# Optimization experiments

Hardware: AMD Instinct MI355X
Metric: run time of the kernel (lower is better)

## Reference

```python
import jax, jax.numpy as jnp
import numpy as np

SIGMA = 1.0

def setup_inputs() -> dict:
    key = jax.random.key(0)
    k1, k2 = jax.random.split(key)
    z = jax.random.normal(k1, (8192, 1024), dtype=jnp.float32)
    expert_keys = jax.random.normal(k2, (4096, 1024), dtype=jnp.float32)
    return {"z": z, "expert_keys": expert_keys}

def reference(z, expert_keys):
    # squared euclidean distances [N, E] = |z|^2 + |e|^2 - 2 z.e
    z_sq = jnp.sum(z * z, axis=-1, keepdims=True)          # [N, 1]
    e_sq = jnp.sum(expert_keys * expert_keys, axis=-1)     # [E]
    dist2 = z_sq + e_sq[None, :] - 2.0 * (z @ expert_keys.T)
    dist2 = jnp.maximum(dist2, 0.0)
    similarity = jnp.exp(-dist2 / (2.0 * SIGMA ** 2))       # [N, E]
    weights = jax.nn.softmax(similarity, axis=-1)            # [N, E]
    weighted_expert = weights @ expert_keys                  # [N, D]
    return (similarity, weighted_expert)
```

## Files before the change

### kernel.cpp

```cpp
#include <hip/hip_runtime.h>
#include <stdint.h>


#define M_TOK 8192
#define N_EXP 4096
#define D_DIM 1024

typedef __attribute__((ext_vector_type(4))) float f32x4;
typedef __attribute__((ext_vector_type(8))) short short8;
typedef __attribute__((ext_vector_type(4))) unsigned short u16x4;
typedef unsigned short u16;
typedef unsigned int u32;

__device__ __forceinline__ u16 f32_to_bf16(float f) {
  u32 u = __builtin_bit_cast(u32, f);
  u += 0x7fff + ((u >> 16) & 1);
  return (u16)(u >> 16);
}

__device__ __forceinline__ void async16(const void* g, void* l) {
  __builtin_amdgcn_global_load_lds((__attribute__((address_space(1))) void*)(g),
                                   (__attribute__((address_space(3))) void*)(l),
                                   16, 0, 0);
}

__global__ __launch_bounds__(256) void prep_convert2(const float* __restrict__ zsrc,
                                                     const float* __restrict__ esrc,
                                                     u16* __restrict__ zdst,
                                                     u16* __restrict__ edst,
                                                     float* __restrict__ zsq,
                                                     float* __restrict__ esq) {
  int row = blockIdx.x;
  const float* src;
  u16* dst;
  float* sq;
  if (row < M_TOK) {
    src = zsrc + (size_t)row * D_DIM;
    dst = zdst + (size_t)row * D_DIM;
    sq = zsq + row;
  } else {
    int r = row - M_TOK;
    src = esrc + (size_t)r * D_DIM;
    dst = edst + (size_t)r * D_DIM;
    sq = esq + r;
  }
  int t = threadIdx.x;
  const float4 v = ((const float4*)src)[t];
  ushort4 h;
  h.x = f32_to_bf16(v.x); h.y = f32_to_bf16(v.y);
  h.z = f32_to_bf16(v.z); h.w = f32_to_bf16(v.w);
  ((ushort4*)dst)[t] = h;
  float p = v.x * v.x + v.y * v.y + v.z * v.z + v.w * v.w;
#pragma unroll
  for (int off = 1; off < 64; off <<= 1) p += __shfl_xor(p, off, 64);
  __shared__ float partial[4];
  if ((t & 63) == 0) partial[t >> 6] = p;
  __syncthreads();
  if (t == 0) *sq = partial[0] + partial[1] + partial[2] + partial[3];
}

__global__ __launch_bounds__(256) void transpose_bf16(const u16* __restrict__ src,
                                                      u16* __restrict__ dst) {
  __shared__ u16 tile[64][65];
  int e0 = blockIdx.x * 64;
  int d0 = blockIdx.y * 64;
  int t = threadIdx.x;
  int lr = t >> 4;
  int lc = (t & 15) * 4;
#pragma unroll
  for (int r8 = 0; r8 < 4; ++r8) {
    int row = lr + r8 * 16;
    ushort4 v = *(const ushort4*)(src + (size_t)(e0 + row) * D_DIM + d0 + lc);
    tile[row][lc + 0] = v.x; tile[row][lc + 1] = v.y;
    tile[row][lc + 2] = v.z; tile[row][lc + 3] = v.w;
  }
  __syncthreads();
#pragma unroll
  for (int r8 = 0; r8 < 4; ++r8) {
    int dl = lr + r8 * 16;
    ushort4 v;
    v.x = tile[lc + 0][dl]; v.y = tile[lc + 1][dl];
    v.z = tile[lc + 2][dl]; v.w = tile[lc + 3][dl];
    *(ushort4*)(dst + (size_t)(d0 + dl) * N_EXP + e0 + lc) = v;
  }
}

__global__ __launch_bounds__(256) void rowsum_reduce(const float* __restrict__ part,
                                                     float* __restrict__ rowsum) {
  int r = blockIdx.x * 256 + threadIdx.x;
  float s = 0.f;
#pragma unroll 8
  for (int j = 0; j < 128; ++j) s += part[(size_t)j * M_TOK + r];
  rowsum[r] = s;
}

template <int EPI>
__global__ __launch_bounds__(512, 4) void gemm_bt(const u16* __restrict__ A,
                                                  const u16* __restrict__ Bt,
                                                  int Mdim, int Ndim, int Kdim,
                                                  float* __restrict__ out, int ldo,
                                                  const float* __restrict__ a_sq,
                                                  const float* __restrict__ b_sq,
                                                  float* __restrict__ rs_part,
                                                  u16* __restrict__ wb,
                                                  const float* __restrict__ scale) {
  constexpr int BM = 128, BN = 128, BK = 64;
  __shared__ __align__(16) u16 smA[2 * BM * BK];
  __shared__ __align__(16) u16 smB[2 * BN * BK];
  __shared__ float inv_rs[BM];

  const int wg = blockIdx.x;
  int m0, n0, ntile = 0;
  if (EPI == 1) {
    const int xcd = wg & 7;
    const int idx = wg >> 3;
    const int sup = idx >> 5;
    const int mloc = (idx & 31) >> 2;
    const int nloc = idx & 3;
    m0 = (xcd * 8 + mloc) * BM;
    ntile = sup * 4 + nloc;
    n0 = ntile * BN;
  } else {
    const int nTilesN = Ndim / BN;
    const int nwg = (Mdim / BM) * nTilesN;
    const int cpx = nwg >> 3;
    const int swz = (wg & 7) * cpx + (wg >> 3);
    m0 = (swz / nTilesN) * BM;
    n0 = (swz % nTilesN) * BN;
  }

  const int t = threadIdx.x;
  const int l = t & 63;
  const int w = t >> 6;
  const int wr = w >> 2;
  const int wc = w & 3;
  const int lr8 = l >> 3;
  const int cswz = (((l & 7) ^ lr8) << 3);
  const int s0 = w * 2, s1 = w * 2 + 1;
  const int str0 = s0 * 8 + lr8, str1 = s1 * 8 + lr8;

  f32x4 acc[4][2];
#pragma unroll
  for (int i = 0; i < 4; ++i)
#pragma unroll
    for (int j = 0; j < 2; ++j) acc[i][j] = (f32x4){0.f, 0.f, 0.f, 0.f};

  const int nIter = Kdim / BK;
  async16(A + (size_t)(m0 + str0) * Kdim + cswz, smA + s0 * 512);
  async16(A + (size_t)(m0 + str1) * Kdim + cswz, smA + s1 * 512);
  async16(Bt + (size_t)(n0 + str0) * Kdim + cswz, smB + s0 * 512);
  async16(Bt + (size_t)(n0 + str1) * Kdim + cswz, smB + s1 * 512);

  if (EPI == 0 && rs_part != nullptr) {
    const int rrow = t >> 2;
    const int q = t & 3;
    float s = 0.f;
#pragma unroll 8
    for (int j = q * 32; j < q * 32 + 32; ++j)
      s += rs_part[(size_t)j * M_TOK + m0 + rrow];
    s += __shfl_xor(s, 1, 64);
    s += __shfl_xor(s, 2, 64);
    if (q == 0) inv_rs[rrow] = 1.0f / s;
  }
  __syncthreads();

  int cur = 0;
  for (int it = 0; it < nIter; ++it) {
    if (it + 1 < nIter) {
      const int k0 = (it + 1) * BK;
      const int nb = (cur ^ 1) * 8192;
      async16(A + (size_t)(m0 + str0) * Kdim + k0 + cswz, smA + nb + s0 * 512);
      async16(A + (size_t)(m0 + str1) * Kdim + k0 + cswz, smA + nb + s1 * 512);
      async16(Bt + (size_t)(n0 + str0) * Kdim + k0 + cswz, smB + nb + s0 * 512);
      async16(Bt + (size_t)(n0 + str1) * Kdim + k0 + cswz, smB + nb + s1 * 512);
    }
    const int cbase = cur * 8192;
#pragma unroll
    for (int ks = 0; ks < 2; ++ks) {
      short8 af[4], bf[2];
      const int lrow = l & 15;
      const int kb = ks * 64 + ((l >> 4) << 4);
#pragma unroll
      for (int mi = 0; mi < 4; ++mi) {
        int row = wr * 64 + mi * 16 + lrow;
        int addr = row * 128 + (kb ^ ((row & 7) << 4));
        af[mi] = *(const short8*)(smA + cbase + (addr >> 1));
      }
#pragma unroll
      for (int ni = 0; ni < 2; ++ni) {
        int row = wc * 32 + ni * 16 + lrow;
        int addr = row * 128 + (kb ^ ((row & 7) << 4));
        bf[ni] = *(const short8*)(smB + cbase + (addr >> 1));
      }
#pragma unroll
      for (int mi = 0; mi < 4; ++mi)
#pragma unroll
        for (int ni = 0; ni < 2; ++ni)
          acc[mi][ni] = __builtin_amdgcn_mfma_f32_16x16x32_bf16(
              bf[ni], af[mi], acc[mi][ni], 0, 0, 0);
    }
    __syncthreads();
    cur ^= 1;
  }

  const int lcol = l & 15;
  const int rgrp = l >> 4;
  if (EPI == 1) {
    float* ldsT = ((float*)smA) + w * (16 * 36);
    const int rr = l >> 3;
    const int c4 = (l & 7) * 4;
    const int slot = ntile * 4 + wc;
#pragma unroll
    for (int mi = 0; mi < 4; ++mi) {
      int grow = m0 + wr * 64 + mi * 16 + lcol;
      float zq = a_sq[grow];
#pragma unroll
      for (int ni = 0; ni < 2; ++ni) {
        int ncol = n0 + wc * 32 + ni * 16 + rgrp * 4;
        f32x4 eqv = *(const f32x4*)(b_sq + ncol);
        f32x4 simv;
#pragma unroll
        for (int r = 0; r < 4; ++r) {
          float dist2 = fmaxf(zq + eqv[r] - 2.0f * acc[mi][ni][r], 0.0f);
          simv[r] = __expf(-0.5f * dist2);
        }
        *(f32x4*)(ldsT + lcol * 36 + ni * 16 + rgrp * 4) = simv;
      }
      asm volatile("s_waitcnt lgkmcnt(0)" ::: "memory");
#pragma unroll
      for (int pass = 0; pass < 2; ++pass) {
        int rrow = pass * 8 + rr;
        f32x4 sv = *(const f32x4*)(ldsT + rrow * 36 + c4);
        int growr = m0 + wr * 64 + mi * 16 + rrow;
        size_t gbase = (size_t)growr * ldo + (n0 + wc * 32 + c4);
        __builtin_nontemporal_store(sv, (f32x4*)(out + gbase));
        f32x4 es;
#pragma unroll
        for (int r = 0; r < 4; ++r) es[r] = __expf(sv[r]);
        if (wb) {
          u16x4 wv;
          wv.x = f32_to_bf16(es[0]); wv.y = f32_to_bf16(es[1]);
          wv.z = f32_to_bf16(es[2]); wv.w = f32_to_bf16(es[3]);
          *(u16x4*)(wb + gbase) = wv;
        }
        float p = es[0] + es[1] + es[2] + es[3];
        p += __shfl_xor(p, 1, 64);
        p += __shfl_xor(p, 2, 64);
        p += __shfl_xor(p, 4, 64);
        if ((l & 7) == 0) rs_part[(size_t)slot * M_TOK + growr] = p;
      }
    }
  } else {
#pragma unroll
    for (int mi = 0; mi < 4; ++mi) {
      int grow = m0 + wr * 64 + mi * 16 + lcol;
      float s;
      if (rs_part != nullptr)      s = inv_rs[wr * 64 + mi * 16 + lcol];
      else if (scale != nullptr)   s = 1.0f / scale[grow];
      else                         s = 1.0f;
#pragma unroll
      for (int ni = 0; ni < 2; ++ni) {
        int ncol = n0 + wc * 32 + ni * 16 + rgrp * 4;
        f32x4 v = acc[mi][ni] * s;
        *(f32x4*)(out + (size_t)grow * ldo + ncol) = v;
      }
    }
  }
}

__global__ __launch_bounds__(256) void weights_kernel(const float* __restrict__ sim,
                                                      const float* __restrict__ rowsum,
                                                      u16* __restrict__ wb) {
  size_t i = ((size_t)blockIdx.x * 256 + threadIdx.x) * 8;
  int row = (int)(i >> 12);
  float inv = 1.0f / rowsum[row];
  float4 a = *(const float4*)(sim + i);
  float4 b = *(const float4*)(sim + i + 4);
  u32 w0 = (u32)f32_to_bf16(__expf(a.x) * inv) | ((u32)f32_to_bf16(__expf(a.y) * inv) << 16);
  u32 w1 = (u32)f32_to_bf16(__expf(a.z) * inv) | ((u32)f32_to_bf16(__expf(a.w) * inv) << 16);
  u32 w2 = (u32)f32_to_bf16(__expf(b.x) * inv) | ((u32)f32_to_bf16(__expf(b.y) * inv) << 16);
  u32 w3 = (u32)f32_to_bf16(__expf(b.z) * inv) | ((u32)f32_to_bf16(__expf(b.w) * inv) << 16);
  uint4 o; o.x = w0; o.y = w1; o.z = w2; o.w = w3;
  *(uint4*)(wb + i) = o;
}

extern "C" void kernel_launch(void* const* d_in, const int* in_sizes, int n_in,
                              void* d_out, int out_size, void* d_ws, size_t ws_size,
                              hipStream_t stream) {
  const float* z = (const float*)d_in[0];
  const float* e = (const float*)d_in[1];
  float* out = (float*)d_out;
  float* sim = out;
  float* wout = out + (size_t)M_TOK * N_EXP;

  char* ws = (char*)d_ws;
  const size_t MB = (size_t)1 << 20;
  const bool fused = ws_size >= 100 * MB + 96 * 1024;

  if (fused) {
    u16* zb  = (u16*)ws;
    u16* eb  = (u16*)(ws + 16 * MB);
    u16* ebT = (u16*)(ws + 24 * MB);
    u16* Wb  = (u16*)(ws + 32 * MB);
    float* rs_part = (float*)(ws + 96 * MB);
    float* z_sq   = (float*)(ws + 100 * MB);
    float* e_sq   = (float*)(ws + 100 * MB + 32768);

    prep_convert2<<<M_TOK + N_EXP, 256, 0, stream>>>(z, e, zb, eb, z_sq, e_sq);
    transpose_bf16<<<dim3(N_EXP / 64, D_DIM / 64), 256, 0, stream>>>(eb, ebT);

    gemm_bt<1><<<(M_TOK / 128) * (N_EXP / 128), 512, 0, stream>>>(
        zb, eb, M_TOK, N_EXP, D_DIM, sim, N_EXP, z_sq, e_sq, rs_part, Wb, nullptr);

    gemm_bt<0><<<(M_TOK / 128) * (D_DIM / 128), 512, 0, stream>>>(
        Wb, ebT, M_TOK, D_DIM, N_EXP, wout, D_DIM, nullptr, nullptr, rs_part,
        nullptr, nullptr);
  } else {
    u16* Wb  = (u16*)ws;
    u16* zb  = (u16*)ws;
    u16* eb  = (u16*)(ws + 64 * MB);
    u16* ebT = (u16*)(ws + 72 * MB);
    float* rs_part = (float*)(ws + 80 * MB);
    float* z_sq   = (float*)(ws + 84 * MB);
    float* e_sq   = (float*)(ws + 84 * MB + 32768);
    float* rowsum = (float*)(ws + 84 * MB + 49152);

    prep_convert2<<<M_TOK + N_EXP, 256, 0, stream>>>(z, e, zb, eb, z_sq, e_sq);
    transpose_bf16<<<dim3(N_EXP / 64, D_DIM / 64), 256, 0, stream>>>(eb, ebT);

    gemm_bt<1><<<(M_TOK / 128) * (N_EXP / 128), 512, 0, stream>>>(
        zb, eb, M_TOK, N_EXP, D_DIM, sim, N_EXP, z_sq, e_sq, rs_part,
        nullptr, nullptr);

    rowsum_reduce<<<M_TOK / 256, 256, 0, stream>>>(rs_part, rowsum);

    weights_kernel<<<(M_TOK * (size_t)N_EXP) / (8 * 256), 256, 0, stream>>>(sim, rowsum, Wb);

    gemm_bt<0><<<(M_TOK / 128) * (D_DIM / 128), 512, 0, stream>>>(
        Wb, ebT, M_TOK, D_DIM, N_EXP, wout, D_DIM, nullptr, nullptr, nullptr,
        nullptr, nullptr);
  }
}
```

Baseline: 188.1 us.

## Make first GEMM persistent, looping over four N tiles per workgroup

Replaces the one-tile-per-workgroup distance/similarity GEMM with a persistent kernel of 512 workgroups. Each workgroup handles four consecutive N tiles for a fixed M tile, with an XCD-aware mapping of M tiles. The first K-slice of the next tile is prefetched into LDS while the current tile's epilogue runs, so loads overlap the exp/store/rowsum work. In exchange, the grid drops from 2048 to 512 workgroups, which may leave less parallelism to hide latency and makes correctness depend on how LDS is reused between the prefetch and the epilogue scratch.

```diff
diff --git a/kernel.cpp b/kernel.cpp
--- a/kernel.cpp
+++ b/kernel.cpp
@@ -94,6 +94,140 @@
   rowsum[r] = s;
 }
 
+__global__ __launch_bounds__(512, 4) void gemm1_persist(const u16* __restrict__ A,
+                                                        const u16* __restrict__ Bt,
+                                                        float* __restrict__ out,
+                                                        const float* __restrict__ a_sq,
+                                                        const float* __restrict__ b_sq,
+                                                        float* __restrict__ rs_part,
+                                                        u16* __restrict__ wb) {
+  constexpr int BM = 128, BN = 128, BK = 64;
+  constexpr int Kdim = D_DIM, ldo = N_EXP, nIter = Kdim / BK;
+  __shared__ __align__(16) u16 smA[2 * BM * BK];
+  __shared__ __align__(16) u16 smB[2 * BN * BK];
+
+  const int wg = blockIdx.x;
+  const int xcd = wg & 7;
+  const int idx = wg >> 3;
+  const int sup = idx >> 3;
+  const int mloc = idx & 7;
+  const int m0 = (xcd * 8 + mloc) * BM;
+
+  const int t = threadIdx.x;
+  const int l = t & 63;
+  const int w = t >> 6;
+  const int wr = w >> 2;
+  const int wc = w & 3;
+  const int lr8 = l >> 3;
+  const int cswz = (((l & 7) ^ lr8) << 3);
+  const int s0 = w * 2, s1 = w * 2 + 1;
+  const int str0 = s0 * 8 + lr8, str1 = s1 * 8 + lr8;
+
+#define STAGE1(n0_, kelem, bufb) do { \
+    async16(A + (size_t)(m0 + str0) * Kdim + (kelem) + cswz, smA + (bufb) + s0 * 512); \
+    async16(A + (size_t)(m0 + str1) * Kdim + (kelem) + cswz, smA + (bufb) + s1 * 512); \
+    async16(Bt + (size_t)((n0_) + str0) * Kdim + (kelem) + cswz, smB + (bufb) + s0 * 512); \
+    async16(Bt + (size_t)((n0_) + str1) * Kdim + (kelem) + cswz, smB + (bufb) + s1 * 512); \
+  } while (0)
+
+  const int lcol = l & 15;
+  const int rgrp = l >> 4;
+  const int rr = l >> 3;
+  const int c4 = (l & 7) * 4;
+  float* ldsT = (w < 4) ? ((float*)(smA + 8192)) + w * (16 * 36)
+                        : ((float*)(smB + 8192)) + (w - 4) * (16 * 36);
+
+  for (int nl = 0; nl < 4; ++nl) {
+    const int ntile = sup * 4 + nl;
+    const int n0 = ntile * BN;
+
+    f32x4 acc[4][2];
+#pragma unroll
+    for (int i = 0; i < 4; ++i)
+#pragma unroll
+      for (int j = 0; j < 2; ++j) acc[i][j] = (f32x4){0.f, 0.f, 0.f, 0.f};
+
+    if (nl == 0) {
+      STAGE1(n0, 0, 0);
+      __syncthreads();
+    }
+    int cur = 0;
+    for (int it = 0; it < nIter; ++it) {
+      if (it + 1 < nIter) STAGE1(n0, (it + 1) * BK, (cur ^ 1) * 8192);
+      const int cbase = cur * 8192;
+#pragma unroll
+      for (int ks = 0; ks < 2; ++ks) {
+        short8 af[4], bf[2];
+        const int lrow = l & 15;
+        const int kb = ks * 64 + ((l >> 4) << 4);
+#pragma unroll
+        for (int mi = 0; mi < 4; ++mi) {
+          int row = wr * 64 + mi * 16 + lrow;
+          int addr = row * 128 + (kb ^ ((row & 7) << 4));
+          af[mi] = *(const short8*)(smA + cbase + (addr >> 1));
+        }
+#pragma unroll
+        for (int ni = 0; ni < 2; ++ni) {
+          int row = wc * 32 + ni * 16 + lrow;
+          int addr = row * 128 + (kb ^ ((row & 7) << 4));
+          bf[ni] = *(const short8*)(smB + cbase + (addr >> 1));
+        }
+#pragma unroll
+        for (int mi = 0; mi < 4; ++mi)
+#pragma unroll
+          for (int ni = 0; ni < 2; ++ni)
+            acc[mi][ni] = __builtin_amdgcn_mfma_f32_16x16x32_bf16(
+                bf[ni], af[mi], acc[mi][ni], 0, 0, 0);
+      }
+      __syncthreads();
+      cur ^= 1;
+    }
+    if (nl < 3) STAGE1(n0 + BN, 0, 0);
+
+    const int slot = ntile * 4 + wc;
+#pragma unroll
+    for (int mi = 0; mi < 4; ++mi) {
+      int grow = m0 + wr * 64 + mi * 16 + lcol;
+      float zq = a_sq[grow];
+#pragma unroll
+      for (int ni = 0; ni < 2; ++ni) {
+        int ncol = n0 + wc * 32 + ni * 16 + rgrp * 4;
+        f32x4 eqv = *(const f32x4*)(b_sq + ncol);
+        f32x4 simv;
+#pragma unroll
+        for (int r = 0; r < 4; ++r) {
+          float dist2 = fmaxf(zq + eqv[r] - 2.0f * acc[mi][ni][r], 0.0f);
+          simv[r] = __expf(-0.5f * dist2);
+        }
+        *(f32x4*)(ldsT + lcol * 36 + ni * 16 + rgrp * 4) = simv;
+      }
+      asm volatile("s_waitcnt lgkmcnt(0)" ::: "memory");
+#pragma unroll
+      for (int pass = 0; pass < 2; ++pass) {
+        int rrow = pass * 8 + rr;
+        f32x4 sv = *(const f32x4*)(ldsT + rrow * 36 + c4);
+        int growr = m0 + wr * 64 + mi * 16 + rrow;
+        size_t gbase = (size_t)growr * ldo + (n0 + wc * 32 + c4);
+        __builtin_nontemporal_store(sv, (f32x4*)(out + gbase));
+        f32x4 es;
+#pragma unroll
+        for (int r = 0; r < 4; ++r) es[r] = __expf(sv[r]);
+        u16x4 wv;
+        wv.x = f32_to_bf16(es[0]); wv.y = f32_to_bf16(es[1]);
+        wv.z = f32_to_bf16(es[2]); wv.w = f32_to_bf16(es[3]);
+        *(u16x4*)(wb + gbase) = wv;
+        float p = es[0] + es[1] + es[2] + es[3];
+        p += __shfl_xor(p, 1, 64);
+        p += __shfl_xor(p, 2, 64);
+        p += __shfl_xor(p, 4, 64);
+        if ((l & 7) == 0) rs_part[(size_t)slot * M_TOK + growr] = p;
+      }
+    }
+    __syncthreads();
+  }
+#undef STAGE1
+}
+
 template <int EPI>
 __global__ __launch_bounds__(512, 4) void gemm_bt(const u16* __restrict__ A,
                                                   const u16* __restrict__ Bt,
@@ -309,8 +443,7 @@
     prep_convert2<<<M_TOK + N_EXP, 256, 0, stream>>>(z, e, zb, eb, z_sq, e_sq);
     transpose_bf16<<<dim3(N_EXP / 64, D_DIM / 64), 256, 0, stream>>>(eb, ebT);
 
-    gemm_bt<1><<<(M_TOK / 128) * (N_EXP / 128), 512, 0, stream>>>(
-        zb, eb, M_TOK, N_EXP, D_DIM, sim, N_EXP, z_sq, e_sq, rs_part, Wb, nullptr);
+    gemm1_persist<<<512, 512, 0, stream>>>(zb, eb, sim, z_sq, e_sq, rs_part, Wb);
 
     gemm_bt<0><<<(M_TOK / 128) * (D_DIM / 128), 512, 0, stream>>>(
         Wb, ebT, M_TOK, D_DIM, N_EXP, wout, D_DIM, nullptr, nullptr, rs_part,
```

After: 216.2 us. 14.9% more time.
